# Optimization experiments

Hardware: AMD Instinct MI355X
Metric: run time of the kernel (lower is better)

## Reference

```python
import jax, jax.numpy as jnp
import numpy as np

IN_F, OUT_F, USER_F = 1024, 512, 512
BSZ, S = 64, 256


def setup_inputs() -> dict:
    key = jax.random.key(0)
    k = jax.random.split(key, 7)
    X_doc = jax.random.normal(k[0], (BSZ, S, IN_F), dtype=jnp.float32)
    X_user = jax.random.normal(k[1], (BSZ, S, USER_F), dtype=jnp.float32)
    # xavier-normal-ish scaling for weights
    Wd = jax.random.normal(k[2], (OUT_F, IN_F), dtype=jnp.float32) * np.sqrt(2.0 / (IN_F + OUT_F))
    bd = jnp.zeros((OUT_F,), dtype=jnp.float32)
    Wu = jax.random.normal(k[3], (OUT_F, USER_F), dtype=jnp.float32) * np.sqrt(2.0 / (USER_F + OUT_F))
    bu = jnp.zeros((OUT_F,), dtype=jnp.float32)
    W = jax.random.normal(k[4], (OUT_F, OUT_F), dtype=jnp.float32) * np.sqrt(1.0 / OUT_F)
    return {"X_doc": X_doc, "X_user": X_user, "Wd": Wd, "bd": bd, "Wu": Wu, "bu": bu, "W": W}


def reference(X_doc, X_user, Wd, bd, Wu, bu, W):
    d = jnp.einsum('bsi,oi->bso', X_doc, Wd) + bd          # (b, s, out)
    u = jnp.einsum('bsi,oi->bso', X_user, Wu) + bu          # (b, s, out)
    d = d * jax.nn.sigmoid(u)
    u = u * jax.nn.sigmoid(d)
    att = jnp.tanh(jnp.einsum('bsd,de,bre->bsr', d, W, u))  # (b, s, s)
    score_d = jax.nn.softmax(att.mean(axis=2), axis=1)[..., None]  # (b, s, 1)
    score_u = jax.nn.softmax(att.mean(axis=1), axis=1)[..., None]  # (b, s, 1)
    attention_d = jnp.sum(score_d * d, axis=1)              # (b, out)
    attention_u = jnp.sum(score_u * u, axis=1)              # (b, out)
    return (attention_d, attention_u)
```

## Files before the change

kernel.cpp:

```cpp
#include <hip/hip_runtime.h>
#include <hip/hip_bf16.h>

#define S_ 256
#define BSZ_ 64
#define IN_F_ 1024
#define OUT_F_ 512
#define USER_F_ 512

typedef short short8 __attribute__((ext_vector_type(8)));
typedef float f32x4 __attribute__((ext_vector_type(4)));

__device__ __forceinline__ ushort f2bf(float f) {
  unsigned u = __float_as_uint(f);
  unsigned r = (u + 0x7FFFu + ((u >> 16) & 1u)) >> 16;
  return (ushort)r;
}
__device__ __forceinline__ float bf2f(unsigned hi16) {
  return __uint_as_float(hi16 << 16);
}
__device__ __forceinline__ float sigf(float x) {
  return 1.f / (1.f + __expf(-x));
}
__device__ __forceinline__ float tanh_safe(float x) {
  float ax = fabsf(x);
  float e = __expf(-2.f * ax);
  float r = (1.f - e) / (1.f + e);
  return copysignf(r, x);
}

__device__ __forceinline__ void gl_lds16(const ushort* g, ushort* l) {
  __builtin_amdgcn_global_load_lds(
      (const __attribute__((address_space(1))) void*)g,
      (__attribute__((address_space(3))) void*)l, 16, 0, 0);
}

__global__ void prep(const float* __restrict__ Xd, const float* __restrict__ Xu,
                     const float* __restrict__ Wd, const float* __restrict__ Wu,
                     const float* __restrict__ W,
                     ushort* __restrict__ Xd_bf, ushort* __restrict__ Xu_bf,
                     ushort* __restrict__ Wd_bf, ushort* __restrict__ Wu_bf,
                     ushort* __restrict__ W_bf, float* __restrict__ rowlog) {
  int i = blockIdx.x * 256 + threadIdx.x;
  if (i < 4194304) {
    float4 v = ((const float4*)Xd)[i];
    ushort4 o; o.x = f2bf(v.x); o.y = f2bf(v.y); o.z = f2bf(v.z); o.w = f2bf(v.w);
    ((ushort4*)Xd_bf)[i] = o;
  } else if (i < 6291456) {
    int j = i - 4194304;
    float4 v = ((const float4*)Xu)[j];
    ushort4 o; o.x = f2bf(v.x); o.y = f2bf(v.y); o.z = f2bf(v.z); o.w = f2bf(v.w);
    ((ushort4*)Xu_bf)[j] = o;
  } else if (i < 6422528) {
    int j = i - 6291456;
    float4 v = ((const float4*)Wd)[j];
    ushort4 o; o.x = f2bf(v.x); o.y = f2bf(v.y); o.z = f2bf(v.z); o.w = f2bf(v.w);
    ((ushort4*)Wd_bf)[j] = o;
  } else if (i < 6488064) {
    int j = i - 6422528;
    float4 v = ((const float4*)Wu)[j];
    ushort4 o; o.x = f2bf(v.x); o.y = f2bf(v.y); o.z = f2bf(v.z); o.w = f2bf(v.w);
    ((ushort4*)Wu_bf)[j] = o;
  } else if (i < 6553600) {
    int j = i - 6488064;
    float4 v = ((const float4*)W)[j];
    ushort4 o; o.x = f2bf(v.x); o.y = f2bf(v.y); o.z = f2bf(v.z); o.w = f2bf(v.w);
    ((ushort4*)W_bf)[j] = o;
  } else {
    int j = i - 6553600;
    ((float4*)rowlog)[j] = float4{0.f, 0.f, 0.f, 0.f};
  }
}

template <int ROWS>
__device__ __forceinline__ void stage_tile(const ushort* __restrict__ g, int K,
                                           ushort* lds, int w, int lane) {
  const int rin = lane >> 3;
  const int c = lane & 7;
#pragma unroll
  for (int i = 0; i < ROWS / 32; ++i) {
    int r = w * (ROWS / 4) + i * 8 + rin;
    int gc = c ^ (r & 7);
    gl_lds16(g + (long)r * K + gc * 8, lds + w * (ROWS / 4) * 64 + i * 512);
  }
}
__device__ __forceinline__ void stage_tile8w(const ushort* __restrict__ g, int K,
                                             ushort* lds, int w, int lane) {
  const int rin = lane >> 3, c = lane & 7;
#pragma unroll
  for (int i = 0; i < 2; ++i) {
    int r = w * 16 + i * 8 + rin;
    int gc = c ^ (r & 7);
    gl_lds16(g + (long)r * K + gc * 8, lds + w * 1024 + i * 512);
  }
}

__device__ __forceinline__ short8 frag(const ushort* lds, int row, int kk, int q) {
  int pc = (kk * 4 + q) ^ (row & 7);
  return *(const short8*)(lds + row * 64 + pc * 8);
}

__device__ __forceinline__ void compute8w(const ushort* As, const ushort* Bs,
                                          f32x4 acc[4][2], int wr, int wc,
                                          int mlane, int q) {
#pragma unroll
  for (int kk = 0; kk < 2; ++kk) {
    short8 af[4], bfr[2];
#pragma unroll
    for (int r = 0; r < 4; ++r) af[r] = frag(As, wr * 64 + r * 16 + mlane, kk, q);
#pragma unroll
    for (int c = 0; c < 2; ++c) bfr[c] = frag(Bs, wc * 32 + c * 16 + mlane, kk, q);
#pragma unroll
    for (int r = 0; r < 4; ++r)
#pragma unroll
      for (int c = 0; c < 2; ++c)
        acc[r][c] = __builtin_amdgcn_mfma_f32_16x16x32_bf16(af[r], bfr[c], acc[r][c], 0, 0, 0);
  }
}
__device__ __forceinline__ void compute4w(const ushort* As, const ushort* Bs,
                                          f32x4 acc[4][4], int wr, int wc,
                                          int mlane, int q) {
#pragma unroll
  for (int kk = 0; kk < 2; ++kk) {
    short8 af[4], bfr[4];
#pragma unroll
    for (int r = 0; r < 4; ++r) af[r] = frag(As, wr * 64 + r * 16 + mlane, kk, q);
#pragma unroll
    for (int c = 0; c < 4; ++c) bfr[c] = frag(Bs, wc * 64 + c * 16 + mlane, kk, q);
#pragma unroll
    for (int r = 0; r < 4; ++r)
#pragma unroll
      for (int c = 0; c < 4; ++c)
        acc[r][c] = __builtin_amdgcn_mfma_f32_16x16x32_bf16(af[r], bfr[c], acc[r][c], 0, 0, 0);
  }
}

#define ACC_ZERO2(a)                            \
  _Pragma("unroll") for (int r = 0; r < 4; ++r) \
  _Pragma("unroll") for (int c = 0; c < 2; ++c) { \
    a[r][c][0] = 0.f; a[r][c][1] = 0.f; a[r][c][2] = 0.f; a[r][c][3] = 0.f; }
#define ACC_ZERO4(a)                            \
  _Pragma("unroll") for (int r = 0; r < 4; ++r) \
  _Pragma("unroll") for (int c = 0; c < 4; ++c) { \
    a[r][c][0] = 0.f; a[r][c][1] = 0.f; a[r][c][2] = 0.f; a[r][c][3] = 0.f; }

template <int NSTEP>
__device__ __forceinline__ void loop8w(const ushort* __restrict__ A,
                                       const ushort* __restrict__ B, int K,
                                       ushort* sm, f32x4 acc[4][2], int w,
                                       int lane, int wr, int wc, int mlane, int q) {
  stage_tile8w(A, K, sm, w, lane);
  stage_tile8w(B, K, sm + 8192, w, lane);
  __syncthreads();
  int cur = 0;
#pragma unroll 1
  for (int k = 0; k < NSTEP; ++k) {
    if (k + 1 < NSTEP) {
      ushort* dst = sm + (cur ^ 1) * 16384;
      stage_tile8w(A + (k + 1) * 64, K, dst, w, lane);
      stage_tile8w(B + (k + 1) * 64, K, dst + 8192, w, lane);
    }
    const ushort* Asc = sm + cur * 16384;
    compute8w(Asc, Asc + 8192, acc, wr, wc, mlane, q);
    __syncthreads();
    cur ^= 1;
  }
}
template <int NSTEP>
__device__ __forceinline__ void loop4w(const ushort* __restrict__ A,
                                       const ushort* __restrict__ B, int K,
                                       ushort* sm, f32x4 acc[4][4], int w,
                                       int lane, int wr, int wc, int mlane, int q) {
  stage_tile<128>(A, K, sm, w, lane);
  stage_tile<128>(B, K, sm + 8192, w, lane);
  __syncthreads();
  int cur = 0;
#pragma unroll 1
  for (int k = 0; k < NSTEP; ++k) {
    if (k + 1 < NSTEP) {
      ushort* dst = sm + (cur ^ 1) * 16384;
      stage_tile<128>(A + (k + 1) * 64, K, dst, w, lane);
      stage_tile<128>(B + (k + 1) * 64, K, dst + 8192, w, lane);
    }
    const ushort* Asc = sm + cur * 16384;
    compute4w(Asc, Asc + 8192, acc, wr, wc, mlane, q);
    __syncthreads();
    cur ^= 1;
  }
}

__global__ __launch_bounds__(512, 4) void gemm_du(
    const ushort* __restrict__ Xd, const ushort* __restrict__ Wd,
    const float* __restrict__ bd,
    const ushort* __restrict__ Xu, const ushort* __restrict__ Wu,
    const float* __restrict__ bu,
    ushort* __restrict__ dg, ushort* __restrict__ ug) {
  __shared__ ushort sm[32768];
  const int i = blockIdx.x;
  const int xcd = i & 7, j = i >> 3;
  const int by = xcd * 16 + (j >> 2), bx = j & 3;
  const int tid = threadIdx.x, lane = tid & 63, w = tid >> 6;
  const int wr = w >> 2, wc = w & 3, mlane = lane & 15, q = lane >> 4;
  const int m0 = by * 128, n0 = bx * 128;

  f32x4 accd[4][2]; ACC_ZERO2(accd);
  loop8w<16>(Xd + (long)m0 * 1024, Wd + (long)n0 * 1024, 1024, sm, accd,
             w, lane, wr, wc, mlane, q);
  f32x4 accu[4][2]; ACC_ZERO2(accu);
  loop8w<8>(Xu + (long)m0 * 512, Wu + (long)n0 * 512, 512, sm, accu,
            w, lane, wr, wc, mlane, q);

#pragma unroll
  for (int c = 0; c < 2; ++c) {
    const int gn = n0 + wc * 32 + c * 16 + mlane;
    const float bdv = bd[gn], buv = bu[gn];
#pragma unroll
    for (int r = 0; r < 4; ++r)
#pragma unroll
      for (int ii = 0; ii < 4; ++ii) {
        const int gm = m0 + wr * 64 + r * 16 + q * 4 + ii;
        const long idx = (long)gm * OUT_F_ + gn;
        float dp = accd[r][c][ii] + bdv;
        float up = accu[r][c][ii] + buv;
        float dgv = dp * sigf(up);
        float ugv = up * sigf(dgv);
        dg[idx] = f2bf(dgv);
        ug[idx] = f2bf(ugv);
      }
  }
}

__global__ __launch_bounds__(256, 2) void gemm_v(
    const ushort* __restrict__ ug, const ushort* __restrict__ Wb,
    ushort* __restrict__ v) {
  __shared__ ushort sm[32768];
  const int i = blockIdx.x;
  const int xcd = i & 7, j = i >> 3;
  const int by = xcd * 16 + (j >> 2), bx = j & 3;
  const int tid = threadIdx.x, lane = tid & 63, w = tid >> 6;
  const int wr = w >> 1, wc = w & 1, mlane = lane & 15, q = lane >> 4;
  const int m0 = by * 128, n0 = bx * 128;

  f32x4 acc[4][4]; ACC_ZERO4(acc);
  loop4w<8>(ug + (long)m0 * 512, Wb + (long)n0 * 512, 512, sm, acc,
            w, lane, wr, wc, mlane, q);
#pragma unroll
  for (int c = 0; c < 4; ++c) {
    const int gn = n0 + wc * 64 + c * 16 + mlane;
#pragma unroll
    for (int r = 0; r < 4; ++r)
#pragma unroll
      for (int ii = 0; ii < 4; ++ii) {
        const int gm = m0 + wr * 64 + r * 16 + q * 4 + ii;
        v[(long)gm * OUT_F_ + gn] = f2bf(acc[r][c][ii]);
      }
  }
}

__global__ __launch_bounds__(256, 2) void att(
    const ushort* __restrict__ dgp, const ushort* __restrict__ v,
    float* __restrict__ rowlog, float* __restrict__ collog) {
  __shared__ ushort sm[32768];
  const int i = blockIdx.x;
  const int xcd = i & 7, j = i >> 3;
  const int b = xcd * 8 + (j >> 2);
  const int mt = (j >> 1) & 1, nt = j & 1;
  const int tid = threadIdx.x, lane = tid & 63, w = tid >> 6;
  const int wr = w >> 1, wc = w & 1, mlane = lane & 15, q = lane >> 4;

  f32x4 acc[4][4]; ACC_ZERO4(acc);
  loop4w<8>(dgp + ((long)b * S_ + mt * 128) * 512,
            v + ((long)b * S_ + nt * 128) * 512, 512, sm, acc,
            w, lane, wr, wc, mlane, q);

  float rs[16], cs[4];
#pragma unroll
  for (int x = 0; x < 16; ++x) rs[x] = 0.f;
#pragma unroll
  for (int c = 0; c < 4; ++c) cs[c] = 0.f;
#pragma unroll
  for (int r = 0; r < 4; ++r)
#pragma unroll
    for (int c = 0; c < 4; ++c)
#pragma unroll
      for (int ii = 0; ii < 4; ++ii) {
        float vv = tanh_safe(acc[r][c][ii]);
        rs[r * 4 + ii] += vv;
        cs[c] += vv;
      }
#pragma unroll
  for (int m = 1; m < 16; m <<= 1)
#pragma unroll
    for (int x = 0; x < 16; ++x) rs[x] += __shfl_xor(rs[x], m, 64);
#pragma unroll
  for (int m = 16; m < 64; m <<= 1)
#pragma unroll
    for (int c = 0; c < 4; ++c) cs[c] += __shfl_xor(cs[c], m, 64);

  const int s0 = mt * 128 + wr * 64;
  const int r0 = nt * 128 + wc * 64;
  if (mlane == 0) {
#pragma unroll
    for (int x = 0; x < 16; ++x)
      atomicAdd(&rowlog[b * S_ + s0 + (x >> 2) * 16 + q * 4 + (x & 3)], rs[x]);
  }
  if (q == 0) {
#pragma unroll
    for (int c = 0; c < 4; ++c)
      atomicAdd(&collog[b * S_ + r0 + c * 16 + mlane], cs[c]);
  }
}

__device__ __forceinline__ float block_max(float v, float* buf, int tid) {
  buf[tid] = v; __syncthreads();
  for (int s = 128; s > 0; s >>= 1) {
    if (tid < s) buf[tid] = fmaxf(buf[tid], buf[tid + s]);
    __syncthreads();
  }
  float r = buf[0]; __syncthreads();
  return r;
}
__device__ __forceinline__ float block_sum(float v, float* buf, int tid) {
  buf[tid] = v; __syncthreads();
  for (int s = 128; s > 0; s >>= 1) {
    if (tid < s) buf[tid] = buf[tid] + buf[tid + s];
    __syncthreads();
  }
  float r = buf[0]; __syncthreads();
  return r;
}

__global__ __launch_bounds__(256) void finalize(
    const float* __restrict__ rowlog, const float* __restrict__ collog,
    const ushort* __restrict__ dg, const ushort* __restrict__ ug,
    float* __restrict__ out) {
  __shared__ float sd[S_], su[S_], buf[S_];
  const int b = blockIdx.x >> 2, oc = blockIdx.x & 3;
  const int tid = threadIdx.x;

  const float rowmean = rowlog[b * S_ + tid] * (1.f / (float)S_);
  const float colmean = collog[b * S_ + tid] * (1.f / (float)S_);

  float md = block_max(rowmean, buf, tid);
  float ed = __expf(rowmean - md);
  float sds = block_sum(ed, buf, tid);
  sd[tid] = ed / sds;
  float mu = block_max(colmean, buf, tid);
  float eu = __expf(colmean - mu);
  float sus = block_sum(eu, buf, tid);
  su[tid] = eu / sus;
  __syncthreads();

  const int o = oc * 128 + (tid & 127);
  const ushort* src = (tid < 128) ? dg : ug;
  const float* sw = (tid < 128) ? sd : su;
  const ushort* p = src + (long)b * (S_ * OUT_F_) + o;
  float a = 0.f;
#pragma unroll 8
  for (int s = 0; s < S_; ++s) a += sw[s] * bf2f((unsigned)p[s * OUT_F_]);
  out[((tid < 128) ? 0 : BSZ_ * OUT_F_) + b * OUT_F_ + o] = a;
}

extern "C" void kernel_launch(void* const* d_in, const int* in_sizes, int n_in,
                              void* d_out, int out_size, void* d_ws, size_t ws_size,
                              hipStream_t stream) {
  (void)in_sizes; (void)n_in; (void)out_size; (void)ws_size;
  const float* Xd = (const float*)d_in[0];
  const float* Xu = (const float*)d_in[1];
  const float* Wd = (const float*)d_in[2];
  const float* bd = (const float*)d_in[3];
  const float* Wu = (const float*)d_in[4];
  const float* bu = (const float*)d_in[5];
  const float* W  = (const float*)d_in[6];
  float* out = (float*)d_out;
  char* ws = (char*)d_ws;

  ushort* Xd_bf  = (ushort*)(ws + 0L);
  ushort* Xu_bf  = (ushort*)(ws + 33554432L);
  ushort* Wd_bf  = (ushort*)(ws + 50331648L);
  ushort* Wu_bf  = (ushort*)(ws + 51380224L);
  ushort* W_bf   = (ushort*)(ws + 51904512L);
  ushort* dg     = (ushort*)(ws + 52428800L);
  ushort* ug     = (ushort*)(ws + 69206016L);
  float*  rowlog = (float*)(ws + 85983232L);
  float*  collog = (float*)(ws + 86048768L);
  ushort* v_buf  = Xd_bf;

  prep<<<25632, 256, 0, stream>>>(Xd, Xu, Wd, Wu, W, Xd_bf, Xu_bf,
                                  Wd_bf, Wu_bf, W_bf, rowlog);

  gemm_du<<<512, dim3(512), 0, stream>>>(Xd_bf, Wd_bf, bd, Xu_bf, Wu_bf, bu, dg, ug);
  gemm_v<<<512, dim3(256), 0, stream>>>(ug, W_bf, v_buf);
  att<<<256, dim3(256), 0, stream>>>(dg, v_buf, rowlog, collog);
  finalize<<<256, dim3(256), 0, stream>>>(rowlog, collog, dg, ug, out);
}
```

Baseline: 210.4 us.

## Fuse fp32-to-bf16 activation conversion into GEMM A-tile loading

New measurement: 222.4 us. +5.7%, slower.

```diff
diff --git a/kernel.cpp b/kernel.cpp
--- a/kernel.cpp
+++ b/kernel.cpp
@@ -34,39 +34,27 @@
       (__attribute__((address_space(3))) void*)l, 16, 0, 0);
 }
 
-__global__ void prep(const float* __restrict__ Xd, const float* __restrict__ Xu,
-                     const float* __restrict__ Wd, const float* __restrict__ Wu,
+__global__ void prep(const float* __restrict__ Wd, const float* __restrict__ Wu,
                      const float* __restrict__ W,
-                     ushort* __restrict__ Xd_bf, ushort* __restrict__ Xu_bf,
                      ushort* __restrict__ Wd_bf, ushort* __restrict__ Wu_bf,
                      ushort* __restrict__ W_bf, float* __restrict__ rowlog) {
   int i = blockIdx.x * 256 + threadIdx.x;
-  if (i < 4194304) {
-    float4 v = ((const float4*)Xd)[i];
+  if (i < 131072) {
+    float4 v = ((const float4*)Wd)[i];
     ushort4 o; o.x = f2bf(v.x); o.y = f2bf(v.y); o.z = f2bf(v.z); o.w = f2bf(v.w);
-    ((ushort4*)Xd_bf)[i] = o;
-  } else if (i < 6291456) {
-    int j = i - 4194304;
-    float4 v = ((const float4*)Xu)[j];
-    ushort4 o; o.x = f2bf(v.x); o.y = f2bf(v.y); o.z = f2bf(v.z); o.w = f2bf(v.w);
-    ((ushort4*)Xu_bf)[j] = o;
-  } else if (i < 6422528) {
-    int j = i - 6291456;
-    float4 v = ((const float4*)Wd)[j];
-    ushort4 o; o.x = f2bf(v.x); o.y = f2bf(v.y); o.z = f2bf(v.z); o.w = f2bf(v.w);
-    ((ushort4*)Wd_bf)[j] = o;
-  } else if (i < 6488064) {
-    int j = i - 6422528;
+    ((ushort4*)Wd_bf)[i] = o;
+  } else if (i < 196608) {
+    int j = i - 131072;
     float4 v = ((const float4*)Wu)[j];
     ushort4 o; o.x = f2bf(v.x); o.y = f2bf(v.y); o.z = f2bf(v.z); o.w = f2bf(v.w);
     ((ushort4*)Wu_bf)[j] = o;
-  } else if (i < 6553600) {
-    int j = i - 6488064;
+  } else if (i < 262144) {
+    int j = i - 196608;
     float4 v = ((const float4*)W)[j];
     ushort4 o; o.x = f2bf(v.x); o.y = f2bf(v.y); o.z = f2bf(v.z); o.w = f2bf(v.w);
     ((ushort4*)W_bf)[j] = o;
   } else {
-    int j = i - 6553600;
+    int j = i - 262144;
     ((float4*)rowlog)[j] = float4{0.f, 0.f, 0.f, 0.f};
   }
 }
@@ -92,6 +80,29 @@
     int gc = c ^ (r & 7);
     gl_lds16(g + (long)r * K + gc * 8, lds + w * 1024 + i * 512);
   }
+}
+
+__device__ __forceinline__ void ldA_f32(const float* __restrict__ X, int K,
+                                        int k, int t, float4 v[4]) {
+  const int r = t >> 2, seg = t & 3;
+  const float4* p = (const float4*)(X + (long)r * K + k * 64 + seg * 16);
+  v[0] = p[0]; v[1] = p[1]; v[2] = p[2]; v[3] = p[3];
+}
+__device__ __forceinline__ void wrA_bf(ushort* lds, int t, const float4 v[4]) {
+  const int r = t >> 2, seg = t & 3;
+  const int cc0 = seg * 2;
+  const int p0 = cc0 ^ (r & 7), p1 = (cc0 + 1) ^ (r & 7);
+  short8 a, b;
+  a[0] = (short)f2bf(v[0].x); a[1] = (short)f2bf(v[0].y);
+  a[2] = (short)f2bf(v[0].z); a[3] = (short)f2bf(v[0].w);
+  a[4] = (short)f2bf(v[1].x); a[5] = (short)f2bf(v[1].y);
+  a[6] = (short)f2bf(v[1].z); a[7] = (short)f2bf(v[1].w);
+  b[0] = (short)f2bf(v[2].x); b[1] = (short)f2bf(v[2].y);
+  b[2] = (short)f2bf(v[2].z); b[3] = (short)f2bf(v[2].w);
+  b[4] = (short)f2bf(v[3].x); b[5] = (short)f2bf(v[3].y);
+  b[6] = (short)f2bf(v[3].z); b[7] = (short)f2bf(v[3].w);
+  *(short8*)(lds + r * 64 + p0 * 8) = a;
+  *(short8*)(lds + r * 64 + p1 * 8) = b;
 }
 
 __device__ __forceinline__ short8 frag(const ushort* lds, int row, int kk, int q) {
@@ -144,23 +155,27 @@
     a[r][c][0] = 0.f; a[r][c][1] = 0.f; a[r][c][2] = 0.f; a[r][c][3] = 0.f; }
 
 template <int NSTEP>
-__device__ __forceinline__ void loop8w(const ushort* __restrict__ A,
-                                       const ushort* __restrict__ B, int K,
-                                       ushort* sm, f32x4 acc[4][2], int w,
-                                       int lane, int wr, int wc, int mlane, int q) {
-  stage_tile8w(A, K, sm, w, lane);
+__device__ __forceinline__ void loop8w_f32A(const float* __restrict__ Xf,
+                                            const ushort* __restrict__ B, int K,
+                                            ushort* sm, f32x4 acc[4][2], int tid,
+                                            int w, int lane, int wr, int wc,
+                                            int mlane, int q) {
+  float4 av[4];
+  ldA_f32(Xf, K, 0, tid, av);
   stage_tile8w(B, K, sm + 8192, w, lane);
+  wrA_bf(sm, tid, av);
   __syncthreads();
   int cur = 0;
 #pragma unroll 1
   for (int k = 0; k < NSTEP; ++k) {
+    ushort* dst = sm + (cur ^ 1) * 16384;
     if (k + 1 < NSTEP) {
-      ushort* dst = sm + (cur ^ 1) * 16384;
-      stage_tile8w(A + (k + 1) * 64, K, dst, w, lane);
+      ldA_f32(Xf, K, k + 1, tid, av);
       stage_tile8w(B + (k + 1) * 64, K, dst + 8192, w, lane);
     }
     const ushort* Asc = sm + cur * 16384;
     compute8w(Asc, Asc + 8192, acc, wr, wc, mlane, q);
+    if (k + 1 < NSTEP) wrA_bf(dst, tid, av);
     __syncthreads();
     cur ^= 1;
   }
@@ -189,9 +204,9 @@
 }
 
 __global__ __launch_bounds__(512, 4) void gemm_du(
-    const ushort* __restrict__ Xd, const ushort* __restrict__ Wd,
+    const float* __restrict__ Xd, const ushort* __restrict__ Wd,
     const float* __restrict__ bd,
-    const ushort* __restrict__ Xu, const ushort* __restrict__ Wu,
+    const float* __restrict__ Xu, const ushort* __restrict__ Wu,
     const float* __restrict__ bu,
     ushort* __restrict__ dg, ushort* __restrict__ ug) {
   __shared__ ushort sm[32768];
@@ -203,11 +218,11 @@
   const int m0 = by * 128, n0 = bx * 128;
 
   f32x4 accd[4][2]; ACC_ZERO2(accd);
-  loop8w<16>(Xd + (long)m0 * 1024, Wd + (long)n0 * 1024, 1024, sm, accd,
-             w, lane, wr, wc, mlane, q);
+  loop8w_f32A<16>(Xd + (long)m0 * 1024, Wd + (long)n0 * 1024, 1024, sm, accd,
+                  tid, w, lane, wr, wc, mlane, q);
   f32x4 accu[4][2]; ACC_ZERO2(accu);
-  loop8w<8>(Xu + (long)m0 * 512, Wu + (long)n0 * 512, 512, sm, accu,
-            w, lane, wr, wc, mlane, q);
+  loop8w_f32A<8>(Xu + (long)m0 * 512, Wu + (long)n0 * 512, 512, sm, accu,
+                 tid, w, lane, wr, wc, mlane, q);
 
 #pragma unroll
   for (int c = 0; c < 2; ++c) {
@@ -374,8 +389,7 @@
   float* out = (float*)d_out;
   char* ws = (char*)d_ws;
 
-  ushort* Xd_bf  = (ushort*)(ws + 0L);
-  ushort* Xu_bf  = (ushort*)(ws + 33554432L);
+  ushort* v_buf  = (ushort*)(ws + 0L);
   ushort* Wd_bf  = (ushort*)(ws + 50331648L);
   ushort* Wu_bf  = (ushort*)(ws + 51380224L);
   ushort* W_bf   = (ushort*)(ws + 51904512L);
@@ -383,12 +397,10 @@
   ushort* ug     = (ushort*)(ws + 69206016L);
   float*  rowlog = (float*)(ws + 85983232L);
   float*  collog = (float*)(ws + 86048768L);
-  ushort* v_buf  = Xd_bf;
-
-  prep<<<25632, 256, 0, stream>>>(Xd, Xu, Wd, Wu, W, Xd_bf, Xu_bf,
-                                  Wd_bf, Wu_bf, W_bf, rowlog);
-
-  gemm_du<<<512, dim3(512), 0, stream>>>(Xd_bf, Wd_bf, bd, Xu_bf, Wu_bf, bu, dg, ug);
+
+  prep<<<1056, 256, 0, stream>>>(Wd, Wu, W, Wd_bf, Wu_bf, W_bf, rowlog);
+
+  gemm_du<<<512, dim3(512), 0, stream>>>(Xd, Wd_bf, bd, Xu, Wu_bf, bu, dg, ug);
   gemm_v<<<512, dim3(256), 0, stream>>>(ug, W_bf, v_buf);
   att<<<256, dim3(256), 0, stream>>>(dg, v_buf, rowlog, collog);
   finalize<<<256, dim3(256), 0, stream>>>(rowlog, collog, dg, ug, out);
```

## Switch gemm_du to 4-wave tiles with finer vmcnt waits and setprio

Applied to the files above, without the earlier changes.

After: 212.2 us. About the same (+0.8%).

```diff
diff --git a/kernel.cpp b/kernel.cpp
--- a/kernel.cpp
+++ b/kernel.cpp
@@ -83,39 +83,12 @@
     gl_lds16(g + (long)r * K + gc * 8, lds + w * (ROWS / 4) * 64 + i * 512);
   }
 }
-__device__ __forceinline__ void stage_tile8w(const ushort* __restrict__ g, int K,
-                                             ushort* lds, int w, int lane) {
-  const int rin = lane >> 3, c = lane & 7;
-#pragma unroll
-  for (int i = 0; i < 2; ++i) {
-    int r = w * 16 + i * 8 + rin;
-    int gc = c ^ (r & 7);
-    gl_lds16(g + (long)r * K + gc * 8, lds + w * 1024 + i * 512);
-  }
-}
 
 __device__ __forceinline__ short8 frag(const ushort* lds, int row, int kk, int q) {
   int pc = (kk * 4 + q) ^ (row & 7);
   return *(const short8*)(lds + row * 64 + pc * 8);
 }
 
-__device__ __forceinline__ void compute8w(const ushort* As, const ushort* Bs,
-                                          f32x4 acc[4][2], int wr, int wc,
-                                          int mlane, int q) {
-#pragma unroll
-  for (int kk = 0; kk < 2; ++kk) {
-    short8 af[4], bfr[2];
-#pragma unroll
-    for (int r = 0; r < 4; ++r) af[r] = frag(As, wr * 64 + r * 16 + mlane, kk, q);
-#pragma unroll
-    for (int c = 0; c < 2; ++c) bfr[c] = frag(Bs, wc * 32 + c * 16 + mlane, kk, q);
-#pragma unroll
-    for (int r = 0; r < 4; ++r)
-#pragma unroll
-      for (int c = 0; c < 2; ++c)
-        acc[r][c] = __builtin_amdgcn_mfma_f32_16x16x32_bf16(af[r], bfr[c], acc[r][c], 0, 0, 0);
-  }
-}
 __device__ __forceinline__ void compute4w(const ushort* As, const ushort* Bs,
                                           f32x4 acc[4][4], int wr, int wc,
                                           int mlane, int q) {
@@ -134,37 +107,11 @@
   }
 }
 
-#define ACC_ZERO2(a)                            \
-  _Pragma("unroll") for (int r = 0; r < 4; ++r) \
-  _Pragma("unroll") for (int c = 0; c < 2; ++c) { \
-    a[r][c][0] = 0.f; a[r][c][1] = 0.f; a[r][c][2] = 0.f; a[r][c][3] = 0.f; }
 #define ACC_ZERO4(a)                            \
   _Pragma("unroll") for (int r = 0; r < 4; ++r) \
   _Pragma("unroll") for (int c = 0; c < 4; ++c) { \
     a[r][c][0] = 0.f; a[r][c][1] = 0.f; a[r][c][2] = 0.f; a[r][c][3] = 0.f; }
 
-template <int NSTEP>
-__device__ __forceinline__ void loop8w(const ushort* __restrict__ A,
-                                       const ushort* __restrict__ B, int K,
-                                       ushort* sm, f32x4 acc[4][2], int w,
-                                       int lane, int wr, int wc, int mlane, int q) {
-  stage_tile8w(A, K, sm, w, lane);
-  stage_tile8w(B, K, sm + 8192, w, lane);
-  __syncthreads();
-  int cur = 0;
-#pragma unroll 1
-  for (int k = 0; k < NSTEP; ++k) {
-    if (k + 1 < NSTEP) {
-      ushort* dst = sm + (cur ^ 1) * 16384;
-      stage_tile8w(A + (k + 1) * 64, K, dst, w, lane);
-      stage_tile8w(B + (k + 1) * 64, K, dst + 8192, w, lane);
-    }
-    const ushort* Asc = sm + cur * 16384;
-    compute8w(Asc, Asc + 8192, acc, wr, wc, mlane, q);
-    __syncthreads();
-    cur ^= 1;
-  }
-}
 template <int NSTEP>
 __device__ __forceinline__ void loop4w(const ushort* __restrict__ A,
                                        const ushort* __restrict__ B, int K,
@@ -172,7 +119,6 @@
                                        int lane, int wr, int wc, int mlane, int q) {
   stage_tile<128>(A, K, sm, w, lane);
   stage_tile<128>(B, K, sm + 8192, w, lane);
-  __syncthreads();
   int cur = 0;
 #pragma unroll 1
   for (int k = 0; k < NSTEP; ++k) {
@@ -180,15 +126,23 @@
       ushort* dst = sm + (cur ^ 1) * 16384;
       stage_tile<128>(A + (k + 1) * 64, K, dst, w, lane);
       stage_tile<128>(B + (k + 1) * 64, K, dst + 8192, w, lane);
+      asm volatile("s_waitcnt vmcnt(8)" ::: "memory");
+    } else {
+      asm volatile("s_waitcnt vmcnt(0)" ::: "memory");
     }
+    __builtin_amdgcn_s_barrier();
+    asm volatile("" ::: "memory");
     const ushort* Asc = sm + cur * 16384;
+    __builtin_amdgcn_s_setprio(1);
     compute4w(Asc, Asc + 8192, acc, wr, wc, mlane, q);
-    __syncthreads();
+    __builtin_amdgcn_s_setprio(0);
+    asm volatile("" ::: "memory");
+    __builtin_amdgcn_s_barrier();
     cur ^= 1;
   }
 }
 
-__global__ __launch_bounds__(512, 4) void gemm_du(
+__global__ __launch_bounds__(256, 2) void gemm_du(
     const ushort* __restrict__ Xd, const ushort* __restrict__ Wd,
     const float* __restrict__ bd,
     const ushort* __restrict__ Xu, const ushort* __restrict__ Wu,
@@ -199,19 +153,19 @@
   const int xcd = i & 7, j = i >> 3;
   const int by = xcd * 16 + (j >> 2), bx = j & 3;
   const int tid = threadIdx.x, lane = tid & 63, w = tid >> 6;
-  const int wr = w >> 2, wc = w & 3, mlane = lane & 15, q = lane >> 4;
+  const int wr = w >> 1, wc = w & 1, mlane = lane & 15, q = lane >> 4;
   const int m0 = by * 128, n0 = bx * 128;
 
-  f32x4 accd[4][2]; ACC_ZERO2(accd);
-  loop8w<16>(Xd + (long)m0 * 1024, Wd + (long)n0 * 1024, 1024, sm, accd,
+  f32x4 accd[4][4]; ACC_ZERO4(accd);
+  loop4w<16>(Xd + (long)m0 * 1024, Wd + (long)n0 * 1024, 1024, sm, accd,
              w, lane, wr, wc, mlane, q);
-  f32x4 accu[4][2]; ACC_ZERO2(accu);
-  loop8w<8>(Xu + (long)m0 * 512, Wu + (long)n0 * 512, 512, sm, accu,
+  f32x4 accu[4][4]; ACC_ZERO4(accu);
+  loop4w<8>(Xu + (long)m0 * 512, Wu + (long)n0 * 512, 512, sm, accu,
             w, lane, wr, wc, mlane, q);
 
 #pragma unroll
-  for (int c = 0; c < 2; ++c) {
-    const int gn = n0 + wc * 32 + c * 16 + mlane;
+  for (int c = 0; c < 4; ++c) {
+    const int gn = n0 + wc * 64 + c * 16 + mlane;
     const float bdv = bd[gn], buv = bu[gn];
 #pragma unroll
     for (int r = 0; r < 4; ++r)
@@ -388,7 +342,7 @@
   prep<<<25632, 256, 0, stream>>>(Xd, Xu, Wd, Wu, W, Xd_bf, Xu_bf,
                                   Wd_bf, Wu_bf, W_bf, rowlog);
 
-  gemm_du<<<512, dim3(512), 0, stream>>>(Xd_bf, Wd_bf, bd, Xu_bf, Wu_bf, bu, dg, ug);
+  gemm_du<<<512, dim3(256), 0, stream>>>(Xd_bf, Wd_bf, bd, Xu_bf, Wu_bf, bu, dg, ug);
   gemm_v<<<512, dim3(256), 0, stream>>>(ug, W_bf, v_buf);
   att<<<256, dim3(256), 0, stream>>>(dg, v_buf, rowlog, collog);
   finalize<<<256, dim3(256), 0, stream>>>(rowlog, collog, dg, ug, out);
```
